# Kernel tuning notes

Measured on AMD Instinct MI355X. Metric: run time of the kernel, lower is better.

## Reference

```python
import jax, jax.numpy as jnp
import numpy as np

N_NODES = 150000
N_EDGES = 2400000
N_GRAPHS = 1024
EPS = 1e-5


def setup_inputs() -> dict:
    key = jax.random.key(0)
    ks = jax.random.split(key, 20)
    x = jax.random.normal(ks[0], (N_NODES, 3), dtype=jnp.float32)
    edge_index = jax.random.randint(ks[1], (2, N_EDGES), 0, N_NODES, dtype=jnp.int64)
    batch = jnp.sort(jax.random.randint(ks[2], (N_NODES,), 0, N_GRAPHS, dtype=jnp.int64))

    def glorot(k, shape):
        fan_in, fan_out = shape[0], shape[1]
        lim = jnp.sqrt(6.0 / (fan_in + fan_out)).astype(jnp.float32)
        return jax.random.uniform(k, shape, jnp.float32, -lim, lim)

    params = dict(
        W1=glorot(ks[3], (3, 32)), b1=jnp.zeros((32,), jnp.float32),
        gn1_w=jnp.ones((32,), jnp.float32), gn1_b=jnp.zeros((32,), jnp.float32), gn1_ms=jnp.ones((32,), jnp.float32),
        W2=glorot(ks[4], (32, 32)), b2=jnp.zeros((32,), jnp.float32),
        gn2_w=jnp.ones((32,), jnp.float32), gn2_b=jnp.zeros((32,), jnp.float32), gn2_ms=jnp.ones((32,), jnp.float32),
        W3=glorot(ks[5], (32, 32)), b3=jnp.zeros((32,), jnp.float32),
        gn3_w=jnp.ones((32,), jnp.float32), gn3_b=jnp.zeros((32,), jnp.float32), gn3_ms=jnp.ones((32,), jnp.float32),
        lin_w=glorot(ks[6], (32, 3)), lin_b=jnp.zeros((3,), jnp.float32),
    )
    return dict(x=x, edge_index=edge_index, batch=batch, **params)


def _gcn_conv(x, W, b, src, dst, dinv_sqrt):
    # PyG GCNConv: h = x @ W; propagate with sym-normalized A + self-loops; + bias
    h = x @ W  # [N, F]
    coef = dinv_sqrt[src] * dinv_sqrt[dst]  # [E]
    msgs = h[src] * coef[:, None]  # [E, F]
    agg = jax.ops.segment_sum(msgs, dst, num_segments=N_NODES)
    agg = agg + (dinv_sqrt * dinv_sqrt)[:, None] * h  # self-loop term
    return agg + b


def _graph_norm(x, batch, counts, weight, bias, mean_scale):
    # PyG GraphNorm: per-graph mean/var with learnable mean_scale
    mean = jax.ops.segment_sum(x, batch, num_segments=N_GRAPHS) / counts[:, None]
    out = x - mean_scale * mean[batch]
    var = jax.ops.segment_sum(out * out, batch, num_segments=N_GRAPHS) / counts[:, None]
    std = jnp.sqrt(var + EPS)
    return weight * out / std[batch] + bias


def reference(x, edge_index, batch,
              W1, b1, gn1_w, gn1_b, gn1_ms,
              W2, b2, gn2_w, gn2_b, gn2_ms,
              W3, b3, gn3_w, gn3_b, gn3_ms,
              lin_w, lin_b):
    src, dst = edge_index[0], edge_index[1]
    # degree over A + I (edge weight 1)
    deg = jax.ops.segment_sum(jnp.ones((N_EDGES,), jnp.float32), dst, num_segments=N_NODES) + 1.0
    dinv_sqrt = jax.lax.rsqrt(deg)
    counts = jax.ops.segment_sum(jnp.ones((N_NODES,), jnp.float32), batch, num_segments=N_GRAPHS)

    x1 = jax.nn.relu(_graph_norm(_gcn_conv(x, W1, b1, src, dst, dinv_sqrt), batch, counts, gn1_w, gn1_b, gn1_ms))
    h2 = _graph_norm(_gcn_conv(x1, W2, b2, src, dst, dinv_sqrt), batch, counts, gn2_w, gn2_b, gn2_ms)
    x2 = jax.nn.relu(h2 + x1)
    h3 = _graph_norm(_gcn_conv(x2, W3, b3, src, dst, dinv_sqrt), batch, counts, gn3_w, gn3_b, gn3_ms)
    x3 = jax.nn.relu(h3 + x2)

    pooled = jax.ops.segment_sum(x3, batch, num_segments=N_GRAPHS) / counts[:, None]  # mean pool
    return pooled @ lin_w + lin_b  # [G, 3]
```

## Files before the change

kernel.cpp:

```cpp
#include <hip/hip_runtime.h>

#define N_NODES 150000
#define N_EDGES 2400000
#define N_GRAPHS 1024
#define F 32
#define EPSV 1e-5f

#define BS 256
#define NB ((N_NODES + BS - 1) / BS)
#define CAP 5120
#define EB 8192
#define NEB ((N_EDGES + EB - 1) / EB)
#define EPT (EB / 256)
#define KPT (CAP / 256)

#define SSH 14
#define NS 10

__device__ __forceinline__ float bflo(unsigned int u) {
    union { unsigned int i; float f; } v; v.i = u << 16; return v.f;
}
__device__ __forceinline__ float bfhi(unsigned int u) {
    union { unsigned int i; float f; } v; v.i = u & 0xffff0000u; return v.f;
}
__device__ __forceinline__ unsigned int f2bf(float f) {
    union { float f; unsigned int i; } v; v.f = f;
    unsigned int r = v.i + 0x7fff + ((v.i >> 16) & 1);
    return r >> 16;
}

__global__ void k_init(const int* __restrict__ batch, int* __restrict__ bucketCur,
                       int* __restrict__ off, float* __restrict__ gstats) {
    int i = blockIdx.x * blockDim.x + threadIdx.x;
    if (i >= N_NODES) return;
    if (i < NB) bucketCur[i] = i * CAP;
    if (i < N_GRAPHS * 9) gstats[i] = 0.f;
    int b = batch[i];
    if (i == 0) {
        for (int g = 0; g <= b; ++g) off[g] = 0;
    } else {
        int pb = batch[i - 1];
        for (int g = pb + 1; g <= b; ++g) off[g] = i;
    }
    if (i == N_NODES - 1) {
        for (int g = b + 1; g <= N_GRAPHS; ++g) off[g] = N_NODES;
    }
}

__global__ __launch_bounds__(256) void k_bin(const int* __restrict__ src,
                                             const int* __restrict__ dst,
                                             int* __restrict__ bucketCur,
                                             unsigned int* __restrict__ binned) {
    __shared__ int h[NB];
    __shared__ int gb[NB];
    int t = threadIdx.x;
    for (int b = t; b < NB; b += 256) h[b] = 0;
    __syncthreads();
    int base = blockIdx.x * EB + t;
    unsigned int key[EPT];
    unsigned int pk[EPT];
#pragma unroll
    for (int k = 0; k < EPT; ++k) {
        int e = base + k * 256;
        if (e < N_EDGES) {
            int d = dst[e];
            int b = d >> 8;
            key[k] = ((unsigned int)(d & 255) << 18) | (unsigned int)src[e];
            unsigned int rk = (unsigned int)atomicAdd(&h[b], 1);
            pk[k] = (rk << 10) | (unsigned int)b;
        } else {
            pk[k] = 0xFFFFFFFFu;
        }
    }
    __syncthreads();
    for (int b = t; b < NB; b += 256) {
        int c = h[b];
        gb[b] = c ? atomicAdd(&bucketCur[b], c) : 0;
    }
    __syncthreads();
#pragma unroll
    for (int k = 0; k < EPT; ++k) {
        if (pk[k] != 0xFFFFFFFFu) {
            unsigned int b = pk[k] & 1023u;
            unsigned int rk = pk[k] >> 10;
            binned[gb[b] + rk] = key[k];
        }
    }
}

__global__ __launch_bounds__(256) void k_csr(const unsigned int* __restrict__ binned,
                                             const int* __restrict__ bucketCur,
                                             const float* __restrict__ x,
                                             unsigned int* __restrict__ rowptr,
                                             float* __restrict__ dinv,
                                             float* __restrict__ xs4,
                                             int* __restrict__ csr) {
    __shared__ int cnt[256 * NS];
    __shared__ int pre[256 * NS];
    __shared__ int sc[256];
    int b = blockIdx.x, t = threadIdx.x;
    int e0 = b * CAP;
    int e1 = bucketCur[b];
#pragma unroll
    for (int s = 0; s < NS; ++s) cnt[t * NS + s] = 0;
    __syncthreads();
    unsigned int kc[KPT];
#pragma unroll
    for (int k = 0; k < KPT; ++k) {
        int e = e0 + t + k * 256;
        if (e < e1) {
            kc[k] = binned[e];
            atomicAdd(&cnt[(kc[k] >> 18) * NS + ((kc[k] & 0x3FFFFu) >> SSH)], 1);
        }
    }
    __syncthreads();
    int run = 0;
#pragma unroll
    for (int s = 0; s < NS; ++s) {
        int c = cnt[t * NS + s];
        pre[t * NS + s] = run;
        run += c;
    }
    int v = run;
    sc[t] = v;
    __syncthreads();
    for (int o = 1; o < 256; o <<= 1) {
        int x2 = (t >= o) ? sc[t - o] : 0;
        __syncthreads();
        sc[t] += x2;
        __syncthreads();
    }
    int excl = sc[t] - v;
#pragma unroll
    for (int s = 0; s < NS; ++s) {
        pre[t * NS + s] += excl;
        cnt[t * NS + s] = 0;
    }
    int gnode = b * BS + t;
    if (gnode < N_NODES) {
        rowptr[gnode] = ((unsigned int)(e0 + excl) << 8) | (unsigned int)min(v, 255);
        float dv = rsqrtf((float)v + 1.0f);
        dinv[gnode] = dv;
        float4 xv;
        xv.x = x[gnode * 3 + 0] * dv;
        xv.y = x[gnode * 3 + 1] * dv;
        xv.z = x[gnode * 3 + 2] * dv;
        xv.w = 0.f;
        ((float4*)xs4)[gnode] = xv;
    }
    __syncthreads();
#pragma unroll
    for (int k = 0; k < KPT; ++k) {
        int e = e0 + t + k * 256;
        if (e < e1) {
            unsigned int key = kc[k];
            int idx = (int)(key >> 18) * NS + (int)((key & 0x3FFFFu) >> SSH);
            int pos = atomicAdd(&cnt[idx], 1);
            csr[e0 + pre[idx] + pos] = (int)(key & 0x3FFFFu);
        }
    }
}

__global__ __launch_bounds__(256, 8) void k_gz(
        const float* __restrict__ xs4, const int* __restrict__ csr,
        const unsigned int* __restrict__ rowptr, const float* __restrict__ dinv,
        const int* __restrict__ batch,
        float* __restrict__ zs4, float* __restrict__ gstats) {
    __shared__ float st[8 * 12];
    __shared__ int gbase_s;
    int t = threadIdx.x;
    for (int i = t; i < 8 * 12; i += 256) st[i] = 0.f;
    if (t == 0) gbase_s = batch[blockIdx.x * 128];
    __syncthreads();

    int gid = blockIdx.x * 256 + t;
    int n = gid >> 1, h = gid & 1;
    float z0 = 0.f, z1 = 0.f, z2 = 0.f;
    if (n < N_NODES) {
        const float4* xv = (const float4*)xs4;
        unsigned int rp = rowptr[n];
        int st0 = (int)(rp >> 8);
        int len = (int)(rp & 255u);
        int half0 = (len + 1) >> 1;
        int e  = h ? (st0 + half0) : st0;
        int e1 = h ? (st0 + len)   : (st0 + half0);
        if (!h) {
            float4 sv = xv[n];
            z0 = sv.x; z1 = sv.y; z2 = sv.z;
        }
        int nch = (e1 - e) >> 2;
        if (nch > 0) {
            int eb = e;
            int a0 = 0, a1 = 0, a2 = 0, a3 = 0;
            float4 d0, d1, d2, d3;
            {
                int i0 = csr[eb], i1 = csr[eb + 1], i2 = csr[eb + 2], i3 = csr[eb + 3];
                d0 = xv[i0]; d1 = xv[i1]; d2 = xv[i2]; d3 = xv[i3];
            }
            if (nch > 1) {
                const int* cp = csr + eb + 4;
                a0 = cp[0]; a1 = cp[1]; a2 = cp[2]; a3 = cp[3];
            }
            for (int ch = 1; ch < nch; ++ch) {
                float4 t0 = xv[a0], t1 = xv[a1], t2 = xv[a2], t3 = xv[a3];
                if (ch + 1 < nch) {
                    const int* cp = csr + eb + 4 * (ch + 1);
                    a0 = cp[0]; a1 = cp[1]; a2 = cp[2]; a3 = cp[3];
                }
                z0 += d0.x + d1.x + d2.x + d3.x;
                z1 += d0.y + d1.y + d2.y + d3.y;
                z2 += d0.z + d1.z + d2.z + d3.z;
                d0 = t0; d1 = t1; d2 = t2; d3 = t3;
            }
            z0 += d0.x + d1.x + d2.x + d3.x;
            z1 += d0.y + d1.y + d2.y + d3.y;
            z2 += d0.z + d1.z + d2.z + d3.z;
            e += nch * 4;
        }
        for (; e < e1; ++e) {
            float4 u = xv[csr[e]];
            z0 += u.x; z1 += u.y; z2 += u.z;
        }
    }
    z0 += __shfl_down(z0, 1);
    z1 += __shfl_down(z1, 1);
    z2 += __shfl_down(z2, 1);
    if (h == 0 && n < N_NODES) {
        float dd = dinv[n];
        z0 *= dd; z1 *= dd; z2 *= dd;
        float4 zv; zv.x = z0; zv.y = z1; zv.z = z2; zv.w = 0.f;
        ((float4*)zs4)[n] = zv;
        int g = batch[n];
        int lg = g - gbase_s;
        if (lg < 8) {
            float* sp = &st[lg * 12];
            atomicAdd(&sp[0], z0);      atomicAdd(&sp[1], z1);
            atomicAdd(&sp[2], z2);      atomicAdd(&sp[3], z0 * z0);
            atomicAdd(&sp[4], z0 * z1); atomicAdd(&sp[5], z0 * z2);
            atomicAdd(&sp[6], z1 * z1); atomicAdd(&sp[7], z1 * z2);
            atomicAdd(&sp[8], z2 * z2);
        } else {
            float* gp = &gstats[g * 9];
            atomicAdd(&gp[0], z0);      atomicAdd(&gp[1], z1);
            atomicAdd(&gp[2], z2);      atomicAdd(&gp[3], z0 * z0);
            atomicAdd(&gp[4], z0 * z1); atomicAdd(&gp[5], z0 * z2);
            atomicAdd(&gp[6], z1 * z1); atomicAdd(&gp[7], z1 * z2);
            atomicAdd(&gp[8], z2 * z2);
        }
    }
    __syncthreads();
    if (t < 72) {
        int slot = t / 9, k = t % 9;
        int g = gbase_s + slot;
        float v = st[slot * 12 + k];
        if (g < N_GRAPHS && v != 0.f) atomicAdd(&gstats[g * 9 + k], v);
    }
}

__global__ __launch_bounds__(256) void k_prep(
        const float* __restrict__ gstats, const int* __restrict__ off,
        const float* __restrict__ W, const float* __restrict__ bias,
        const float* __restrict__ gw, const float* __restrict__ gms,
        float* __restrict__ mvA, float* __restrict__ scA) {
    int gid = blockIdx.x * 256 + threadIdx.x;
    if (gid >= N_GRAPHS * F) return;
    int g = gid >> 5, f = gid & 31;
    float rc = 1.0f / (float)(off[g + 1] - off[g]);
    const float* sp = &gstats[g * 9];
    float S0 = sp[0], S1 = sp[1], S2 = sp[2];
    float m00 = sp[3], m01 = sp[4], m02 = sp[5], m11 = sp[6], m12 = sp[7], m22 = sp[8];
    float w0 = W[0 * F + f], w1 = W[1 * F + f], w2 = W[2 * F + f];
    float b = bias[f];
    float sy = w0 * S0 + w1 * S1 + w2 * S2;
    float m = sy * rc + b;
    float q = w0 * w0 * m00 + w1 * w1 * m11 + w2 * w2 * m22
            + 2.f * (w0 * w1 * m01 + w0 * w2 * m02 + w1 * w2 * m12);
    float Ey2 = q * rc + 2.f * b * (sy * rc) + b * b;
    float mv = gms[f] * m;
    float var = Ey2 - 2.f * mv * m + mv * mv;
    mvA[gid] = mv;
    scA[gid] = gw[f] * rsqrtf(var + EPSV);
}

__global__ __launch_bounds__(256) void k_n1(
        const float* __restrict__ zs4, const int* __restrict__ batch,
        const float* __restrict__ dinv,
        const float* __restrict__ W, const float* __restrict__ bias,
        const float* __restrict__ gb,
        const float* __restrict__ mvA, const float* __restrict__ scA,
        unsigned short* __restrict__ xh) {
    int gid = blockIdx.x * 256 + threadIdx.x;
    int n = gid >> 3, c = gid & 7;
    if (n >= N_NODES) return;
    float4 zv = ((const float4*)zs4)[n];
    float z0 = zv.x, z1 = zv.y, z2 = zv.z;
    int g = batch[n];
    float dd = dinv[n];
    float4 w0 = ((const float4*)(W + 0 * F))[c];
    float4 w1 = ((const float4*)(W + 1 * F))[c];
    float4 w2 = ((const float4*)(W + 2 * F))[c];
    float4 y  = ((const float4*)bias)[c];
    y.x += z0 * w0.x + z1 * w1.x + z2 * w2.x;
    y.y += z0 * w0.y + z1 * w1.y + z2 * w2.y;
    y.z += z0 * w0.z + z1 * w1.z + z2 * w2.z;
    y.w += z0 * w0.w + z1 * w1.w + z2 * w2.w;
    float4 mv = ((const float4*)mvA)[g * 8 + c];
    float4 sc = ((const float4*)scA)[g * 8 + c];
    float4 bb = ((const float4*)gb)[c];
    float4 o;
    o.x = fmaxf((y.x - mv.x) * sc.x + bb.x, 0.f);
    o.y = fmaxf((y.y - mv.y) * sc.y + bb.y, 0.f);
    o.z = fmaxf((y.z - mv.z) * sc.z + bb.z, 0.f);
    o.w = fmaxf((y.w - mv.w) * sc.w + bb.w, 0.f);
    uint2 hp;
    hp.x = f2bf(o.x * dd) | (f2bf(o.y * dd) << 16);
    hp.y = f2bf(o.z * dd) | (f2bf(o.w * dd) << 16);
    ((uint2*)xh)[n * 8 + c] = hp;
}

#define GAT_CONSUME(U)                                  \
    acc[0] += bflo(U.x); acc[1] += bfhi(U.x);           \
    acc[2] += bflo(U.y); acc[3] += bfhi(U.y);           \
    acc[4] += bflo(U.z); acc[5] += bfhi(U.z);           \
    acc[6] += bflo(U.w); acc[7] += bfhi(U.w);

__global__ __launch_bounds__(256, 8) void k_gat32(
        const unsigned short* __restrict__ xh, const int* __restrict__ csr,
        const unsigned int* __restrict__ rowptr, const float* __restrict__ dinv,
        const float* __restrict__ W, const float* __restrict__ bias,
        float* __restrict__ y) {
    __shared__ float Ws[F * F];
    __shared__ float bs[F];
    __shared__ float Zs[64 * 36];
    int t = threadIdx.x;
    ((float4*)Ws)[t] = ((const float4*)W)[t];
    if (t < F) bs[t] = bias[t];
    __syncthreads();

    int gid = blockIdx.x * 256 + t;
    int n = gid >> 2, c = gid & 3, ln = t >> 2;
    bool act = (n < N_NODES);
    float acc[8];
    if (act) {
        const uint4* xr = (const uint4*)xh;
        uint4 us = xr[n * 4 + c];
        acc[0] = bflo(us.x); acc[1] = bfhi(us.x);
        acc[2] = bflo(us.y); acc[3] = bfhi(us.y);
        acc[4] = bflo(us.z); acc[5] = bfhi(us.z);
        acc[6] = bflo(us.w); acc[7] = bfhi(us.w);
        unsigned int rp = rowptr[n];
        int eb = (int)(rp >> 8);
        int len = (int)(rp & 255u);
        int e1 = eb + len;
        int nch = len >> 2;
        int e = eb;
        if (nch > 0) {
            int a0 = 0, a1 = 0, a2 = 0, a3 = 0;
            uint4 d0, d1, d2, d3;
            {
                int i0 = csr[eb], i1 = csr[eb + 1], i2 = csr[eb + 2], i3 = csr[eb + 3];
                d0 = xr[i0 * 4 + c]; d1 = xr[i1 * 4 + c];
                d2 = xr[i2 * 4 + c]; d3 = xr[i3 * 4 + c];
            }
            if (nch > 1) {
                const int* cp = csr + eb + 4;
                a0 = cp[0]; a1 = cp[1]; a2 = cp[2]; a3 = cp[3];
            }
            for (int ch = 1; ch < nch; ++ch) {
                uint4 t0 = xr[a0 * 4 + c], t1 = xr[a1 * 4 + c];
                uint4 t2 = xr[a2 * 4 + c], t3 = xr[a3 * 4 + c];
                if (ch + 1 < nch) {
                    const int* cp = csr + eb + 4 * (ch + 1);
                    a0 = cp[0]; a1 = cp[1]; a2 = cp[2]; a3 = cp[3];
                }
                GAT_CONSUME(d0) GAT_CONSUME(d1) GAT_CONSUME(d2) GAT_CONSUME(d3)
                d0 = t0; d1 = t1; d2 = t2; d3 = t3;
            }
            GAT_CONSUME(d0) GAT_CONSUME(d1) GAT_CONSUME(d2) GAT_CONSUME(d3)
            e = eb + nch * 4;
        }
        for (; e < e1; ++e) {
            int s0 = csr[e];
            uint4 u0 = xr[s0 * 4 + c];
            GAT_CONSUME(u0)
        }
        float dd = dinv[n];
#pragma unroll
        for (int j = 0; j < 8; ++j) acc[j] *= dd;
    } else {
#pragma unroll
        for (int j = 0; j < 8; ++j) acc[j] = 0.f;
    }
    *(float4*)&Zs[ln * 36 + c * 8]     = *(float4*)&acc[0];
    *(float4*)&Zs[ln * 36 + c * 8 + 4] = *(float4*)&acc[4];
    __syncthreads();

    if (act) {
        const float* zrow = &Zs[ln * 36];
        float4 o0 = ((const float4*)bs)[c * 2];
        float4 o1 = ((const float4*)bs)[c * 2 + 1];
#pragma unroll
        for (int k = 0; k < F; ++k) {
            float zk = zrow[k];
            float4 w0 = ((const float4*)&Ws[k * F])[c * 2];
            float4 w1 = ((const float4*)&Ws[k * F])[c * 2 + 1];
            o0.x += zk * w0.x; o0.y += zk * w0.y; o0.z += zk * w0.z; o0.w += zk * w0.w;
            o1.x += zk * w1.x; o1.y += zk * w1.y; o1.z += zk * w1.z; o1.w += zk * w1.w;
        }
        ((float4*)y)[n * 8 + c * 2]     = o0;
        ((float4*)y)[n * 8 + c * 2 + 1] = o1;
    }
}

__global__ __launch_bounds__(256) void k_gn2(
        const float* agg, const float* __restrict__ zs4,
        const int* __restrict__ off,
        const float* __restrict__ W1, const float* __restrict__ b1,
        const float* __restrict__ gn1b,
        const float* __restrict__ mvA, const float* __restrict__ scA,
        const float* __restrict__ gw, const float* __restrict__ gb,
        const float* __restrict__ gms, const float* __restrict__ dinv,
        unsigned short* __restrict__ xh, float* outp) {
    __shared__ float red1[256], red2[256];
    __shared__ float mv_s[F], sc_s[F];
    int g = blockIdx.x;
    int i0 = off[g], i1 = off[g + 1];
    float rc = 1.0f / (float)(i1 - i0);
    int t = threadIdx.x;
    int f = t & 31, r0 = t >> 5;

    float s = 0.f, q = 0.f;
    for (int n = i0 + r0; n < i1; n += 8) {
        float v = agg[n * F + f];
        s += v; q += v * v;
    }
    red1[t] = s; red2[t] = q; __syncthreads();
    if (t < 128) { red1[t] += red1[t + 128]; red2[t] += red2[t + 128]; } __syncthreads();
    if (t < 64)  { red1[t] += red1[t + 64];  red2[t] += red2[t + 64];  } __syncthreads();
    if (t < 32) {
        float sm = (red1[t] + red1[t + 32]) * rc;
        float sq = (red2[t] + red2[t + 32]) * rc;
        float mv = gms[t] * sm;
        float var = sq - mv * (2.f * sm - mv);
        mv_s[t] = mv;
        sc_s[t] = gw[t] * rsqrtf(var + EPSV);
    }
    __syncthreads();

    float w0r = W1[0 * F + f], w1r = W1[1 * F + f], w2r = W1[2 * F + f];
    float b1f = b1[f], gb1f = gn1b[f];
    float mv1 = mvA[g * F + f], sc1 = scA[g * F + f];

    float w = sc_s[f], mv = mv_s[f], bb = gb[f];
    for (int n = i0 + r0; n < i1; n += 8) {
        float4 zv = ((const float4*)zs4)[n];
        float y1 = b1f + zv.x * w0r + zv.y * w1r + zv.z * w2r;
        float x1 = fmaxf((y1 - mv1) * sc1 + gb1f, 0.f);
        float y = (agg[n * F + f] - mv) * w + bb + x1;
        y = fmaxf(y, 0.f);
        outp[n * F + f] = y;
        xh[n * F + f] = (unsigned short)f2bf(y * dinv[n]);
    }
}

__global__ __launch_bounds__(256) void k_gnfin(
        const float* __restrict__ agg, const float* __restrict__ res,
        const int* __restrict__ off,
        const float* __restrict__ gw, const float* __restrict__ gb,
        const float* __restrict__ gms,
        const float* __restrict__ lin_w, const float* __restrict__ lin_b,
        float* __restrict__ outp) {
    __shared__ float red1[256], red2[256];
    __shared__ float mv_s[F], sc_s[F], pooled_s[F];
    int g = blockIdx.x;
    int i0 = off[g], i1 = off[g + 1];
    float cnt = (float)(i1 - i0);
    float rc = 1.0f / cnt;
    int t = threadIdx.x;
    int f = t & 31, r0 = t >> 5;

    float s = 0.f, q = 0.f;
    for (int n = i0 + r0; n < i1; n += 8) {
        float v = agg[n * F + f];
        s += v; q += v * v;
    }
    red1[t] = s; red2[t] = q; __syncthreads();
    if (t < 128) { red1[t] += red1[t + 128]; red2[t] += red2[t + 128]; } __syncthreads();
    if (t < 64)  { red1[t] += red1[t + 64];  red2[t] += red2[t + 64];  } __syncthreads();
    if (t < 32) {
        float sm = (red1[t] + red1[t + 32]) * rc;
        float sq = (red2[t] + red2[t + 32]) * rc;
        float mv = gms[t] * sm;
        float var = sq - mv * (2.f * sm - mv);
        mv_s[t] = mv;
        sc_s[t] = gw[t] * rsqrtf(var + EPSV);
    }
    __syncthreads();

    float w = sc_s[f], mv = mv_s[f], bb = gb[f];
    float ps = 0.f;
    for (int n = i0 + r0; n < i1; n += 8) {
        float yv = (agg[n * F + f] - mv) * w + bb + res[n * F + f];
        ps += fmaxf(yv, 0.f);
    }
    __syncthreads();
    red1[t] = ps; __syncthreads();
    if (t < 128) red1[t] += red1[t + 128]; __syncthreads();
    if (t < 64)  red1[t] += red1[t + 64];  __syncthreads();
    if (t < 32) { red1[t] += red1[t + 32]; pooled_s[t] = red1[t] * rc; }
    __syncthreads();
    if (t < 3) {
        float o = lin_b[t];
#pragma unroll
        for (int f2 = 0; f2 < F; ++f2) o += pooled_s[f2] * lin_w[f2 * 3 + t];
        outp[g * 3 + t] = o;
    }
}

extern "C" void kernel_launch(void* const* d_in, const int* in_sizes, int n_in,
                              void* d_out, int out_size, void* d_ws, size_t ws_size,
                              hipStream_t stream) {
    const float* x      = (const float*)d_in[0];
    const int*   ei     = (const int*)d_in[1];
    const int*   batch  = (const int*)d_in[2];
    const float* W1     = (const float*)d_in[3];
    const float* b1     = (const float*)d_in[4];
    const float* gn1w   = (const float*)d_in[5];
    const float* gn1b   = (const float*)d_in[6];
    const float* gn1ms  = (const float*)d_in[7];
    const float* W2     = (const float*)d_in[8];
    const float* b2     = (const float*)d_in[9];
    const float* gn2w   = (const float*)d_in[10];
    const float* gn2b   = (const float*)d_in[11];
    const float* gn2ms  = (const float*)d_in[12];
    const float* W3     = (const float*)d_in[13];
    const float* b3     = (const float*)d_in[14];
    const float* gn3w   = (const float*)d_in[15];
    const float* gn3b   = (const float*)d_in[16];
    const float* gn3ms  = (const float*)d_in[17];
    const float* lin_w  = (const float*)d_in[18];
    const float* lin_b  = (const float*)d_in[19];
    float* out = (float*)d_out;

    const int* srcp = ei;
    const int* dstp = ei + N_EDGES;

    char* ws = (char*)d_ws;
    size_t p = 0;
    auto alloc = [&](size_t bytes) {
        size_t r = p; p += (bytes + 511) & ~(size_t)511; return r;
    };
    int*   off       = (int*)  (ws + alloc(sizeof(int) * (N_GRAPHS + 1)));
    int*   bucketCur = (int*)  (ws + alloc(sizeof(int) * NB));
    unsigned int* rowptr = (unsigned int*)(ws + alloc(sizeof(unsigned int) * N_NODES));
    float* dinv      = (float*)(ws + alloc(sizeof(float) * N_NODES));
    float* xs4       = (float*)(ws + alloc(sizeof(float) * N_NODES * 4));
    float* zs4       = (float*)(ws + alloc(sizeof(float) * N_NODES * 4));
    float* gstats    = (float*)(ws + alloc(sizeof(float) * N_GRAPHS * 9));
    float* mvA       = (float*)(ws + alloc(sizeof(float) * N_GRAPHS * F));
    float* scA       = (float*)(ws + alloc(sizeof(float) * N_GRAPHS * F));
    unsigned int* binned = (unsigned int*)(ws + alloc(sizeof(unsigned int) * NB * CAP));
    int*   csr       = (int*)  (ws + alloc(sizeof(int) * NB * CAP));
    float* A         = (float*)(ws + alloc(sizeof(float) * N_NODES * F));
    float* B         = (float*)(ws + alloc(sizeof(float) * N_NODES * F));
    unsigned short* xh = (unsigned short*)binned;
    (void)ws_size; (void)n_in; (void)in_sizes; (void)out_size;

    const int TB = 256;
    dim3 blk(TB);
    int ngrid  = (N_NODES + TB - 1) / TB;
    int ggrid2 = (N_NODES * 2 + TB - 1) / TB;
    int ggrid8 = (N_NODES * 8 + TB - 1) / TB;
    int ggrid4 = (N_NODES * 4 + TB - 1) / TB;

    k_init<<<ngrid, blk, 0, stream>>>(batch, bucketCur, off, gstats);
    k_bin <<<NEB, blk, 0, stream>>>(srcp, dstp, bucketCur, binned);
    k_csr <<<NB, blk, 0, stream>>>(binned, bucketCur, x, rowptr, dinv, xs4, csr);

    k_gz  <<<ggrid2, blk, 0, stream>>>(xs4, csr, rowptr, dinv, batch, zs4, gstats);
    k_prep<<<(N_GRAPHS * F + TB - 1) / TB, blk, 0, stream>>>(
        gstats, off, W1, b1, gn1w, gn1ms, mvA, scA);
    k_n1  <<<ggrid8, blk, 0, stream>>>(zs4, batch, dinv, W1, b1, gn1b, mvA, scA, xh);

    k_gat32<<<ggrid4, blk, 0, stream>>>(xh, csr, rowptr, dinv, W2, b2, B);
    k_gn2<<<N_GRAPHS, blk, 0, stream>>>(
        B, zs4, off, W1, b1, gn1b, mvA, scA,
        gn2w, gn2b, gn2ms, dinv, xh, B);

    k_gat32<<<ggrid4, blk, 0, stream>>>(xh, csr, rowptr, dinv, W3, b3, A);
    k_gnfin<<<N_GRAPHS, blk, 0, stream>>>(A, B, off, gn3w, gn3b, gn3ms,
                                          lin_w, lin_b, out);
}
```

Baseline: 296.1 us.

## Use 8 lanes per node in gather kernel with deeper prefetch pipeline

The gather+matmul kernel now assigns 8 threads per node, each loading a uint2 (4 bf16 features) instead of 4 threads each loading a uint4. The gather loop is also deepened to keep two chunks of neighbour rows in flight plus prefetched indices. This doubles thread-level parallelism and memory requests in flight for the random-access gather, and halves per-thread registers and matmul work. The costs are twice as many threads doing redundant index loads and narrower per-lane memory transactions.

```diff
diff --git a/kernel.cpp b/kernel.cpp
--- a/kernel.cpp
+++ b/kernel.cpp
@@ -318,11 +318,9 @@
     ((uint2*)xh)[n * 8 + c] = hp;
 }
 
-#define GAT_CONSUME(U)                                  \
+#define GAT_CONSUME2(U)                                 \
     acc[0] += bflo(U.x); acc[1] += bfhi(U.x);           \
-    acc[2] += bflo(U.y); acc[3] += bfhi(U.y);           \
-    acc[4] += bflo(U.z); acc[5] += bfhi(U.z);           \
-    acc[6] += bflo(U.w); acc[7] += bfhi(U.w);
+    acc[2] += bflo(U.y); acc[3] += bfhi(U.y);
 
 __global__ __launch_bounds__(256, 8) void k_gat32(
         const unsigned short* __restrict__ xh, const int* __restrict__ csr,
@@ -331,23 +329,21 @@
         float* __restrict__ y) {
     __shared__ float Ws[F * F];
     __shared__ float bs[F];
-    __shared__ float Zs[64 * 36];
+    __shared__ float Zs[32 * 36];
     int t = threadIdx.x;
     ((float4*)Ws)[t] = ((const float4*)W)[t];
     if (t < F) bs[t] = bias[t];
     __syncthreads();
 
     int gid = blockIdx.x * 256 + t;
-    int n = gid >> 2, c = gid & 3, ln = t >> 2;
+    int n = gid >> 3, c = gid & 7, ln = t >> 3;
     bool act = (n < N_NODES);
-    float acc[8];
+    float acc[4];
     if (act) {
-        const uint4* xr = (const uint4*)xh;
-        uint4 us = xr[n * 4 + c];
+        const uint2* xr = (const uint2*)xh;
+        uint2 us = xr[n * 8 + c];
         acc[0] = bflo(us.x); acc[1] = bfhi(us.x);
         acc[2] = bflo(us.y); acc[3] = bfhi(us.y);
-        acc[4] = bflo(us.z); acc[5] = bfhi(us.z);
-        acc[6] = bflo(us.w); acc[7] = bfhi(us.w);
         unsigned int rp = rowptr[n];
         int eb = (int)(rp >> 8);
         int len = (int)(rp & 255u);
@@ -356,59 +352,63 @@
         int e = eb;
         if (nch > 0) {
             int a0 = 0, a1 = 0, a2 = 0, a3 = 0;
-            uint4 d0, d1, d2, d3;
+            uint2 d0, d1, d2, d3, f0, f1, f2, f3;
             {
                 int i0 = csr[eb], i1 = csr[eb + 1], i2 = csr[eb + 2], i3 = csr[eb + 3];
-                d0 = xr[i0 * 4 + c]; d1 = xr[i1 * 4 + c];
-                d2 = xr[i2 * 4 + c]; d3 = xr[i3 * 4 + c];
+                d0 = xr[i0 * 8 + c]; d1 = xr[i1 * 8 + c];
+                d2 = xr[i2 * 8 + c]; d3 = xr[i3 * 8 + c];
             }
             if (nch > 1) {
-                const int* cp = csr + eb + 4;
+                int i0 = csr[eb + 4], i1 = csr[eb + 5], i2 = csr[eb + 6], i3 = csr[eb + 7];
+                f0 = xr[i0 * 8 + c]; f1 = xr[i1 * 8 + c];
+                f2 = xr[i2 * 8 + c]; f3 = xr[i3 * 8 + c];
+            }
+            if (nch > 2) {
+                const int* cp = csr + eb + 8;
                 a0 = cp[0]; a1 = cp[1]; a2 = cp[2]; a3 = cp[3];
             }
-            for (int ch = 1; ch < nch; ++ch) {
-                uint4 t0 = xr[a0 * 4 + c], t1 = xr[a1 * 4 + c];
-                uint4 t2 = xr[a2 * 4 + c], t3 = xr[a3 * 4 + c];
+            for (int ch = 2; ch < nch; ++ch) {
+                uint2 t0 = xr[a0 * 8 + c], t1 = xr[a1 * 8 + c];
+                uint2 t2 = xr[a2 * 8 + c], t3 = xr[a3 * 8 + c];
                 if (ch + 1 < nch) {
                     const int* cp = csr + eb + 4 * (ch + 1);
                     a0 = cp[0]; a1 = cp[1]; a2 = cp[2]; a3 = cp[3];
                 }
-                GAT_CONSUME(d0) GAT_CONSUME(d1) GAT_CONSUME(d2) GAT_CONSUME(d3)
-                d0 = t0; d1 = t1; d2 = t2; d3 = t3;
-            }
-            GAT_CONSUME(d0) GAT_CONSUME(d1) GAT_CONSUME(d2) GAT_CONSUME(d3)
+                GAT_CONSUME2(d0) GAT_CONSUME2(d1) GAT_CONSUME2(d2) GAT_CONSUME2(d3)
+                d0 = f0; d1 = f1; d2 = f2; d3 = f3;
+                f0 = t0; f1 = t1; f2 = t2; f3 = t3;
+            }
+            GAT_CONSUME2(d0) GAT_CONSUME2(d1) GAT_CONSUME2(d2) GAT_CONSUME2(d3)
+            if (nch > 1) {
+                GAT_CONSUME2(f0) GAT_CONSUME2(f1) GAT_CONSUME2(f2) GAT_CONSUME2(f3)
+            }
             e = eb + nch * 4;
         }
         for (; e < e1; ++e) {
             int s0 = csr[e];
-            uint4 u0 = xr[s0 * 4 + c];
-            GAT_CONSUME(u0)
+            uint2 u0 = xr[s0 * 8 + c];
+            GAT_CONSUME2(u0)
         }
         float dd = dinv[n];
 #pragma unroll
-        for (int j = 0; j < 8; ++j) acc[j] *= dd;
+        for (int j = 0; j < 4; ++j) acc[j] *= dd;
     } else {
 #pragma unroll
-        for (int j = 0; j < 8; ++j) acc[j] = 0.f;
-    }
-    *(float4*)&Zs[ln * 36 + c * 8]     = *(float4*)&acc[0];
-    *(float4*)&Zs[ln * 36 + c * 8 + 4] = *(float4*)&acc[4];
+        for (int j = 0; j < 4; ++j) acc[j] = 0.f;
+    }
+    *(float4*)&Zs[ln * 36 + c * 4] = *(float4*)&acc[0];
     __syncthreads();
 
     if (act) {
         const float* zrow = &Zs[ln * 36];
-        float4 o0 = ((const float4*)bs)[c * 2];
-        float4 o1 = ((const float4*)bs)[c * 2 + 1];
+        float4 o0 = ((const float4*)bs)[c];
 #pragma unroll
         for (int k = 0; k < F; ++k) {
             float zk = zrow[k];
-            float4 w0 = ((const float4*)&Ws[k * F])[c * 2];
-            float4 w1 = ((const float4*)&Ws[k * F])[c * 2 + 1];
+            float4 w0 = ((const float4*)&Ws[k * F])[c];
             o0.x += zk * w0.x; o0.y += zk * w0.y; o0.z += zk * w0.z; o0.w += zk * w0.w;
-            o1.x += zk * w1.x; o1.y += zk * w1.y; o1.z += zk * w1.z; o1.w += zk * w1.w;
-        }
-        ((float4*)y)[n * 8 + c * 2]     = o0;
-        ((float4*)y)[n * 8 + c * 2 + 1] = o1;
+        }
+        ((float4*)y)[n * 8 + c] = o0;
     }
 }
 
@@ -571,7 +571,6 @@
     int ngrid  = (N_NODES + TB - 1) / TB;
     int ggrid2 = (N_NODES * 2 + TB - 1) / TB;
     int ggrid8 = (N_NODES * 8 + TB - 1) / TB;
-    int ggrid4 = (N_NODES * 4 + TB - 1) / TB;
 
     k_init<<<ngrid, blk, 0, stream>>>(batch, bucketCur, off, gstats);
     k_bin <<<NEB, blk, 0, stream>>>(srcp, dstp, bucketCur, binned);
@@ -582,12 +581,12 @@
         gstats, off, W1, b1, gn1w, gn1ms, mvA, scA);
     k_n1  <<<ggrid8, blk, 0, stream>>>(zs4, batch, dinv, W1, b1, gn1b, mvA, scA, xh);
 
-    k_gat32<<<ggrid4, blk, 0, stream>>>(xh, csr, rowptr, dinv, W2, b2, B);
+    k_gat32<<<ggrid8, blk, 0, stream>>>(xh, csr, rowptr, dinv, W2, b2, B);
     k_gn2<<<N_GRAPHS, blk, 0, stream>>>(
         B, zs4, off, W1, b1, gn1b, mvA, scA,
         gn2w, gn2b, gn2ms, dinv, xh, B);
 
-    k_gat32<<<ggrid4, blk, 0, stream>>>(xh, csr, rowptr, dinv, W3, b3, A);
+    k_gat32<<<ggrid8, blk, 0, stream>>>(xh, csr, rowptr, dinv, W3, b3, A);
     k_gnfin<<<N_GRAPHS, blk, 0, stream>>>(A, B, off, gn3w, gn3b, gn3ms,
                                           lin_w, lin_b, out);
 }
```

Result: no change. 298.4 us (+0.8%).
